# Kernel optimization log

Measured on AMD Instinct MI355X. Metric: run time of the kernel, lower is better.

Reference implementation:

```python
import jax, jax.numpy as jnp
import numpy as np

# PyTorch LSTM gate order: i, f, g, o. Dropout layers are identity in eval mode.

def _lstm_step(w_ih, w_hh, b):
    def step(carry, xt):
        h, c = carry
        g = xt @ w_ih.T + h @ w_hh.T + b
        i, f, gg, o = jnp.split(g, 4, axis=-1)
        c = jax.nn.sigmoid(f) * c + jax.nn.sigmoid(i) * jnp.tanh(gg)
        h = jax.nn.sigmoid(o) * jnp.tanh(c)
        return (h, c), h
    return step


def bilstm(x, wf_ih, wf_hh, bf_ih, bf_hh, wb_ih, wb_hh, bb_ih, bb_hh):
    # x: [B, T, D] -> out: [B, T, 2H]
    B = x.shape[0]
    H = wf_hh.shape[1]
    xt = jnp.swapaxes(x, 0, 1)  # [T, B, D]
    init = (jnp.zeros((B, H), x.dtype), jnp.zeros((B, H), x.dtype))
    _, hf = jax.lax.scan(_lstm_step(wf_ih, wf_hh, bf_ih + bf_hh), init, xt)
    _, hb = jax.lax.scan(_lstm_step(wb_ih, wb_hh, bb_ih + bb_hh), init, xt[::-1])
    hb = hb[::-1]
    return jnp.swapaxes(jnp.concatenate([hf, hb], axis=-1), 0, 1)


def setup_inputs() -> dict:
    key = jax.random.key(0)
    ks = iter(jax.random.split(key, 64))
    d = {"x": jax.random.normal(next(ks), (1024, 1024, 8), jnp.float32)}
    layer_dims = [(16, 20), (40, 20), (40, 10), (20, 10)]
    for li, (din, H) in enumerate(layer_dims, start=1):
        for dr in ("f", "b"):
            d[f"w{li}{dr}_ih"] = 0.1 * jax.random.normal(next(ks), (4 * H, din), jnp.float32)
            d[f"w{li}{dr}_hh"] = 0.1 * jax.random.normal(next(ks), (4 * H, H), jnp.float32)
            d[f"b{li}{dr}_ih"] = 0.1 * jax.random.normal(next(ks), (4 * H,), jnp.float32)
            d[f"b{li}{dr}_hh"] = 0.1 * jax.random.normal(next(ks), (4 * H,), jnp.float32)
    d["fc_w"] = 0.1 * jax.random.normal(next(ks), (1, 20), jnp.float32)
    d["fc_b"] = 0.1 * jax.random.normal(next(ks), (1,), jnp.float32)
    return d


def reference(x,
              w1f_ih, w1f_hh, b1f_ih, b1f_hh, w1b_ih, w1b_hh, b1b_ih, b1b_hh,
              w2f_ih, w2f_hh, b2f_ih, b2f_hh, w2b_ih, w2b_hh, b2b_ih, b2b_hh,
              w3f_ih, w3f_hh, b3f_ih, b3f_hh, w3b_ih, w3b_hh, b3b_ih, b3b_hh,
              w4f_ih, w4f_hh, b4f_ih, b4f_hh, w4b_ih, w4b_hh, b4b_ih, b4b_hh,
              fc_w, fc_b):
    # lag-1 concat: [B,T,8] -> [B,T,16]
    x_lag = jnp.concatenate([jnp.zeros_like(x[:, :1, :]), x[:, :-1, :]], axis=1)
    h = jnp.concatenate([x, x_lag], axis=2)
    h = bilstm(h, w1f_ih, w1f_hh, b1f_ih, b1f_hh, w1b_ih, w1b_hh, b1b_ih, b1b_hh)
    h = bilstm(h, w2f_ih, w2f_hh, b2f_ih, b2f_hh, w2b_ih, w2b_hh, b2b_ih, b2b_hh)
    h = bilstm(h, w3f_ih, w3f_hh, b3f_ih, b3f_hh, w3b_ih, w3b_hh, b3b_ih, b3b_hh)
    h = bilstm(h, w4f_ih, w4f_hh, b4f_ih, b4f_hh, w4b_ih, w4b_hh, b4b_ih, b4b_hh)
    h = h[:, -1, :]  # [B, 20]
    return jax.nn.sigmoid(h @ fc_w.T + fc_b)
```

## Files before the change

### kernel.cpp

```cpp
#include <hip/hip_runtime.h>
#include <hip/hip_fp16.h>
#include <stdint.h>

#define B_TOTAL 1024
#define T_TOTAL 1024
#define LOG2E 1.44269504088896f

typedef _Float16 f16x2 __attribute__((ext_vector_type(2)));

__device__ __forceinline__ float dot2acc(uint32_t xw, f16x2 w, float acc) {
#if __has_builtin(__builtin_amdgcn_fdot2)
    return __builtin_amdgcn_fdot2(__builtin_bit_cast(f16x2, xw), w, acc, false);
#else
    f16x2 xv = __builtin_bit_cast(f16x2, xw);
    return acc + (float)xv.x * (float)w.x + (float)xv.y * (float)w.y;
#endif
}

__device__ __forceinline__ uint32_t packf2(float a, float b) {
    f16x2 t;
    t.x = (_Float16)a;
    t.y = (_Float16)b;
    return __builtin_bit_cast(uint32_t, t);
}

__device__ __forceinline__ float sigm_(float z) {
    float e = __builtin_amdgcn_exp2f(-LOG2E * z);
    return __builtin_amdgcn_rcpf(1.0f + e);
}
__device__ __forceinline__ float tanh_(float z) {
    float e = __builtin_amdgcn_exp2f((2.0f * LOG2E) * z);
    float r = __builtin_amdgcn_rcpf(1.0f + e);
    return __builtin_fmaf(-2.0f, r, 1.0f);
}

__device__ __forceinline__ void wavebar() {
#if __has_builtin(__builtin_amdgcn_wave_barrier)
    __builtin_amdgcn_wave_barrier();
#endif
}

template <int DIN, int H, bool LAYER1, bool STORE_ALL>
__global__ void __launch_bounds__(64)
__attribute__((amdgpu_waves_per_eu(1, 1))) lstm_scan(
    const float* __restrict__ x,
    const __half* __restrict__ inbuf,
    const float* __restrict__ wihf, const float* __restrict__ whhf,
    const float* __restrict__ bihf, const float* __restrict__ bhhf,
    const float* __restrict__ wihb, const float* __restrict__ whhb,
    const float* __restrict__ bihb, const float* __restrict__ bhhb,
    __half* __restrict__ outbuf,
    float* __restrict__ lasth)
{
    constexpr int GPW   = 64 / H;
    constexpr int ND    = DIN / 2;
    constexpr int NH    = H / 2;
    constexpr int HS_DW = (H == 20) ? 12 : 8;

    const int dir  = blockIdx.y;
    const int lane = threadIdx.x;
    const int g    = lane / H;
    const int j    = lane - g * H;
    const int b    = blockIdx.x * GPW + g;
    const bool valid = (g < GPW) && (b < B_TOTAL);
    const int bs   = valid ? b : (B_TOTAL - 1);

    const float* w_ih = dir ? wihb : wihf;
    const float* w_hh = dir ? whhb : whhf;
    const float* b_ih = dir ? bihb : bihf;
    const float* b_hh = dir ? bhhb : bhhf;

    __shared__ uint32_t hsm[GPW + 1][HS_DW];

    f16x2 wih2[4][ND];
    f16x2 whh2[4][NH];
    float bias[4];
#pragma unroll
    for (int q = 0; q < 4; ++q) {
        const int r = q * H + j;
#pragma unroll
        for (int d = 0; d < ND; ++d) {
            f16x2 t;
            t.x = (_Float16)w_ih[r * DIN + 2 * d];
            t.y = (_Float16)w_ih[r * DIN + 2 * d + 1];
            wih2[q][d] = t;
        }
#pragma unroll
        for (int k = 0; k < NH; ++k) {
            f16x2 t;
            t.x = (_Float16)w_hh[r * H + 2 * k];
            t.y = (_Float16)w_hh[r * H + 2 * k + 1];
            whh2[q][k] = t;
        }
        bias[q] = b_ih[r] + b_hh[r];
    }

    const int tstep = dir ? -1 : 1;
    int tt = dir ? (T_TOTAL - 1) : 0;

    __half* op = nullptr;
    ptrdiff_t opstep = 0;
    if constexpr (STORE_ALL) {
        op = outbuf + (size_t)tt * (B_TOTAL * 2 * H) + (size_t)bs * (2 * H) + dir * H + j;
        opstep = (ptrdiff_t)tstep * (B_TOTAL * 2 * H);
    }

    float c = 0.0f;
    float hlast = 0.0f;
    ((__half*)&hsm[g][0])[j] = __float2half(0.0f);
    wavebar();

    auto tail = [&](const uint32_t* hd, float a0, float a1, float a2, float a3) {
#pragma unroll
        for (int k = 0; k < NH; ++k) {
            a0 = dot2acc(hd[k], whh2[0][k], a0);
            a1 = dot2acc(hd[k], whh2[1][k], a1);
            a2 = dot2acc(hd[k], whh2[2][k], a2);
            a3 = dot2acc(hd[k], whh2[3][k], a3);
        }
        const float iv = sigm_(a0);
        const float fv = sigm_(a1);
        const float gv = tanh_(a2);
        const float ov = sigm_(a3);
        c = __builtin_fmaf(fv, c, iv * gv);
        const float h = ov * tanh_(c);
        ((__half*)&hsm[g][0])[j] = __float2half(h);
        wavebar();
        if constexpr (STORE_ALL) {
            if (valid) *op = __float2half(h);
            op += opstep;
        } else {
            hlast = h;
        }
        tt += tstep;
    };

    if constexpr (LAYER1) {
        const float* xrow = x + (size_t)bs * (T_TOTAL * 8);
        uint32_t xcur[4], xlag[4];
        {
            const float4* p = (const float4*)(xrow + (size_t)tt * 8);
            float4 u0 = p[0], u1 = p[1];
            xcur[0] = packf2(u0.x, u0.y); xcur[1] = packf2(u0.z, u0.w);
            xcur[2] = packf2(u1.x, u1.y); xcur[3] = packf2(u1.z, u1.w);
            if (dir) {
                const float4* q = (const float4*)(xrow + (size_t)(tt - 1) * 8);
                float4 v0 = q[0], v1 = q[1];
                xlag[0] = packf2(v0.x, v0.y); xlag[1] = packf2(v0.z, v0.w);
                xlag[2] = packf2(v1.x, v1.y); xlag[3] = packf2(v1.z, v1.w);
            } else {
#pragma unroll
                for (int d = 0; d < 4; ++d) xlag[d] = 0u;
            }
        }

        for (int t = 0; t < T_TOTAL; ++t) {
            uint32_t hd[NH];
#pragma unroll
            for (int k = 0; k < NH; ++k) hd[k] = hsm[g][k];

            float a0 = bias[0], a1 = bias[1], a2 = bias[2], a3 = bias[3];
#pragma unroll
            for (int d = 0; d < 4; ++d) {
                a0 = dot2acc(xcur[d], wih2[0][d], a0);
                a1 = dot2acc(xcur[d], wih2[1][d], a1);
                a2 = dot2acc(xcur[d], wih2[2][d], a2);
                a3 = dot2acc(xcur[d], wih2[3][d], a3);
            }
#pragma unroll
            for (int d = 0; d < 4; ++d) {
                a0 = dot2acc(xlag[d], wih2[0][4 + d], a0);
                a1 = dot2acc(xlag[d], wih2[1][4 + d], a1);
                a2 = dot2acc(xlag[d], wih2[2][4 + d], a2);
                a3 = dot2acc(xlag[d], wih2[3][4 + d], a3);
            }

            const int li = dir ? (tt - 2) : (tt + 1);
            const bool ld = (li >= 0) && (li < T_TOTAL);
            float4 n0 = {0, 0, 0, 0}, n1 = {0, 0, 0, 0};
            if (ld) {
                const float4* p = (const float4*)(xrow + (size_t)li * 8);
                n0 = p[0];
                n1 = p[1];
            }

            tail(hd, a0, a1, a2, a3);

            uint32_t np[4] = {packf2(n0.x, n0.y), packf2(n0.z, n0.w),
                              packf2(n1.x, n1.y), packf2(n1.z, n1.w)};
            if (dir == 0) {
#pragma unroll
                for (int d = 0; d < 4; ++d) { xlag[d] = xcur[d]; xcur[d] = np[d]; }
            } else {
#pragma unroll
                for (int d = 0; d < 4; ++d) {
                    xcur[d] = xlag[d];
                    xlag[d] = ld ? np[d] : 0u;
                }
            }
        }
    } else {
        const ptrdiff_t ipstep = (ptrdiff_t)tstep * (B_TOTAL * ND);
        const uint32_t* ip = (const uint32_t*)inbuf + (size_t)tt * (B_TOTAL * ND) + (size_t)bs * ND;

        uint32_t xb[4][ND];
#pragma unroll
        for (int s = 0; s < 3; ++s) {
#pragma unroll
            for (int d = 0; d < ND; ++d) xb[s][d] = ip[d];
            ip += ipstep;
        }

        auto step = [&](const uint32_t* xc, uint32_t* xn, bool pf) {
            uint32_t hd[NH];
#pragma unroll
            for (int k = 0; k < NH; ++k) hd[k] = hsm[g][k];

            float a0 = bias[0], a1 = bias[1], a2 = bias[2], a3 = bias[3];
#pragma unroll
            for (int d = 0; d < ND; ++d) {
                a0 = dot2acc(xc[d], wih2[0][d], a0);
                a1 = dot2acc(xc[d], wih2[1][d], a1);
                a2 = dot2acc(xc[d], wih2[2][d], a2);
                a3 = dot2acc(xc[d], wih2[3][d], a3);
            }
            if (pf) {
#pragma unroll
                for (int d = 0; d < ND; ++d) xn[d] = ip[d];
                ip += ipstep;
            }
            tail(hd, a0, a1, a2, a3);
        };

        for (int t = 0; t < T_TOTAL; t += 4) {
            step(xb[0], xb[3], t + 3 < T_TOTAL);
            step(xb[1], xb[0], t + 4 < T_TOTAL);
            step(xb[2], xb[1], t + 5 < T_TOTAL);
            step(xb[3], xb[2], t + 6 < T_TOTAL);
        }
    }

    if constexpr (!STORE_ALL) {
        if (valid) lasth[b * H + j] = hlast;
    }
}

__global__ void final_kernel(const __half* __restrict__ l3out,
                             const float* __restrict__ hf4,
                             const float* __restrict__ w_ih,
                             const float* __restrict__ b_ih,
                             const float* __restrict__ b_hh,
                             const float* __restrict__ fc_w,
                             const float* __restrict__ fc_b,
                             float* __restrict__ out)
{
    const int b = blockIdx.x * blockDim.x + threadIdx.x;
    if (b >= B_TOTAL) return;

    float in4[20];
    const __half* p = l3out + (size_t)(T_TOTAL - 1) * (B_TOTAL * 20) + (size_t)b * 20;
#pragma unroll
    for (int i = 0; i < 20; ++i) in4[i] = __half2float(p[i]);

    float z = fc_b[0];
#pragma unroll
    for (int k = 0; k < 10; ++k) z += fc_w[k] * hf4[b * 10 + k];

#pragma unroll
    for (int k = 0; k < 10; ++k) {
        float gi = b_ih[k]      + b_hh[k];
        float gg = b_ih[20 + k] + b_hh[20 + k];
        float go = b_ih[30 + k] + b_hh[30 + k];
#pragma unroll
        for (int i = 0; i < 20; ++i) {
            const float xi = in4[i];
            gi += w_ih[k * 20 + i]        * xi;
            gg += w_ih[(20 + k) * 20 + i] * xi;
            go += w_ih[(30 + k) * 20 + i] * xi;
        }
        const float cc = sigm_(gi) * tanh_(gg);
        const float hb = sigm_(go) * tanh_(cc);
        z += fc_w[10 + k] * hb;
    }
    out[b] = sigm_(z);
}

extern "C" void kernel_launch(void* const* d_in, const int* in_sizes, int n_in,
                              void* d_out, int out_size, void* d_ws, size_t ws_size,
                              hipStream_t stream) {
    const float* x = (const float*)d_in[0];
    auto W = [&](int li, int dr, int k) -> const float* {
        return (const float*)d_in[1 + (li - 1) * 8 + dr * 4 + k];
    };
    const float* fc_w = (const float*)d_in[33];
    const float* fc_b = (const float*)d_in[34];
    float* out = (float*)d_out;

    __half* buf0 = (__half*)d_ws;
    __half* buf1 = buf0 + (size_t)T_TOTAL * B_TOTAL * 40;
    float* hf4 = (float*)(buf1 + (size_t)T_TOTAL * B_TOTAL * 40);

    lstm_scan<16, 20, true, true><<<dim3(342, 2, 1), 64, 0, stream>>>(
        x, nullptr,
        W(1,0,0), W(1,0,1), W(1,0,2), W(1,0,3),
        W(1,1,0), W(1,1,1), W(1,1,2), W(1,1,3),
        buf0, nullptr);

    lstm_scan<40, 20, false, true><<<dim3(342, 2, 1), 64, 0, stream>>>(
        nullptr, buf0,
        W(2,0,0), W(2,0,1), W(2,0,2), W(2,0,3),
        W(2,1,0), W(2,1,1), W(2,1,2), W(2,1,3),
        buf1, nullptr);

    lstm_scan<40, 10, false, true><<<dim3(171, 2, 1), 64, 0, stream>>>(
        nullptr, buf1,
        W(3,0,0), W(3,0,1), W(3,0,2), W(3,0,3),
        W(3,1,0), W(3,1,1), W(3,1,2), W(3,1,3),
        buf0, nullptr);

    lstm_scan<20, 10, false, false><<<dim3(171, 1, 1), 64, 0, stream>>>(
        nullptr, buf0,
        W(4,0,0), W(4,0,1), W(4,0,2), W(4,0,3),
        W(4,0,0), W(4,0,1), W(4,0,2), W(4,0,3),
        nullptr, hf4);

    final_kernel<<<dim3(4, 1, 1), 256, 0, stream>>>(
        buf0, hf4, W(4,1,0), W(4,1,2), W(4,1,3), fc_w, fc_b, out);
}
```

Measured before the change: 1.739 ms.

## Stage LSTM inputs through double-buffered LDS chunks with coalesced block loads

Replaces the per-lane strided global loads of each timestep's input with chunked cooperative loads. The whole wave fetches CHUNK timesteps into registers, writes them to a double-buffered shared-memory tile mid-chunk, and each lane reads its row from LDS one step ahead. The aim is coalesced global traffic and global load latency hidden off the serial recurrence. It also keeps weights as packed uint32 pinned with empty asm. This adds LDS usage, extra registers for the staging buffer, and indexing arithmetic inside the critical loop.

```diff
diff --git a/kernel.cpp b/kernel.cpp
--- a/kernel.cpp
+++ b/kernel.cpp
@@ -8,12 +8,14 @@
 
 typedef _Float16 f16x2 __attribute__((ext_vector_type(2)));
 
-__device__ __forceinline__ float dot2acc(uint32_t xw, f16x2 w, float acc) {
+__device__ __forceinline__ float dot2w(uint32_t xw, uint32_t ww, float acc) {
 #if __has_builtin(__builtin_amdgcn_fdot2)
-    return __builtin_amdgcn_fdot2(__builtin_bit_cast(f16x2, xw), w, acc, false);
+    return __builtin_amdgcn_fdot2(__builtin_bit_cast(f16x2, xw),
+                                  __builtin_bit_cast(f16x2, ww), acc, false);
 #else
     f16x2 xv = __builtin_bit_cast(f16x2, xw);
-    return acc + (float)xv.x * (float)w.x + (float)xv.y * (float)w.y;
+    f16x2 wv = __builtin_bit_cast(f16x2, ww);
+    return acc + (float)xv.x * (float)wv.x + (float)xv.y * (float)wv.y;
 #endif
 }
 
@@ -52,10 +54,16 @@
     __half* __restrict__ outbuf,
     float* __restrict__ lasth)
 {
-    constexpr int GPW   = 64 / H;
-    constexpr int ND    = DIN / 2;
-    constexpr int NH    = H / 2;
-    constexpr int HS_DW = (H == 20) ? 12 : 8;
+    constexpr int GPW    = 64 / H;
+    constexpr int ND     = DIN / 2;
+    constexpr int NH     = H / 2;
+    constexpr int HS_DW  = (H == 20) ? 12 : 8;
+    constexpr int CHUNK  = (GPW == 3) ? 16 : 8;
+    constexpr int NCHUNK = T_TOTAL / CHUNK;
+    constexpr int NDX    = LAYER1 ? 4 : ND;
+    constexpr int XROWS  = LAYER1 ? (CHUNK + 1) : CHUNK;
+    constexpr int XWORDS = XROWS * GPW * NDX;
+    constexpr int NLOAD  = (XWORDS + 63) / 64;
 
     const int dir  = blockIdx.y;
     const int lane = threadIdx.x;
@@ -70,30 +78,89 @@
     const float* b_ih = dir ? bihb : bihf;
     const float* b_hh = dir ? bhhb : bhhf;
 
+    __shared__ uint32_t xsm[2 * XWORDS];
     __shared__ uint32_t hsm[GPW + 1][HS_DW];
 
-    f16x2 wih2[4][ND];
-    f16x2 whh2[4][NH];
+    uint32_t wih2[4][ND];
+    uint32_t whh2[4][NH];
     float bias[4];
 #pragma unroll
     for (int q = 0; q < 4; ++q) {
         const int r = q * H + j;
 #pragma unroll
-        for (int d = 0; d < ND; ++d) {
-            f16x2 t;
-            t.x = (_Float16)w_ih[r * DIN + 2 * d];
-            t.y = (_Float16)w_ih[r * DIN + 2 * d + 1];
-            wih2[q][d] = t;
-        }
-#pragma unroll
-        for (int k = 0; k < NH; ++k) {
-            f16x2 t;
-            t.x = (_Float16)w_hh[r * H + 2 * k];
-            t.y = (_Float16)w_hh[r * H + 2 * k + 1];
-            whh2[q][k] = t;
-        }
+        for (int d = 0; d < ND; ++d)
+            wih2[q][d] = packf2(w_ih[r * DIN + 2 * d], w_ih[r * DIN + 2 * d + 1]);
+#pragma unroll
+        for (int k = 0; k < NH; ++k)
+            whh2[q][k] = packf2(w_hh[r * H + 2 * k], w_hh[r * H + 2 * k + 1]);
         bias[q] = b_ih[r] + b_hh[r];
     }
+#pragma unroll
+    for (int q = 0; q < 4; ++q) {
+#pragma unroll
+        for (int d = 0; d < ND; ++d) asm volatile("" : "+v"(wih2[q][d]));
+#pragma unroll
+        for (int k = 0; k < NH; ++k) asm volatile("" : "+v"(whh2[q][k]));
+        asm volatile("" : "+v"(bias[q]));
+    }
+
+    uint32_t greg[NLOAD];
+
+    auto stage_load = [&](int c) {
+        const int sbase = c * CHUNK;
+#pragma unroll
+        for (int i = 0; i < NLOAD; ++i) {
+            const int idx = lane + 64 * i;
+            uint32_t v = 0;
+            if (idx < XWORDS) {
+                const int row = idx / (GPW * NDX);
+                const int rem = idx - row * (GPW * NDX);
+                const int r   = rem / NDX;
+                const int d   = rem - r * NDX;
+                const int br  = blockIdx.x * GPW + r;
+                int t;
+                if constexpr (LAYER1)
+                    t = dir ? (T_TOTAL - 1 - sbase) - row : (sbase - 1) + row;
+                else
+                    t = dir ? (T_TOTAL - 1) - (sbase + row) : sbase + row;
+                if (t >= 0 && t < T_TOTAL && br < B_TOTAL) {
+                    if constexpr (LAYER1) {
+                        const float2 p = ((const float2*)(x + (size_t)br * (T_TOTAL * 8) +
+                                                          (size_t)t * 8))[d];
+                        v = packf2(p.x, p.y);
+                    } else {
+                        v = ((const uint32_t*)inbuf)[(size_t)t * (B_TOTAL * ND) +
+                                                     (size_t)br * ND + d];
+                    }
+                }
+            }
+            greg[i] = v;
+        }
+    };
+    auto stage_write = [&](int buf) {
+#pragma unroll
+        for (int i = 0; i < NLOAD; ++i) {
+            const int idx = lane + 64 * i;
+            if (idx < XWORDS) xsm[buf * XWORDS + idx] = greg[i];
+        }
+    };
+
+    auto xread = [&](int buf, int row, uint32_t* dst) {
+        const uint32_t* p = &xsm[buf * XWORDS + row * (GPW * NDX) + g * NDX];
+        if constexpr (NDX % 4 == 0) {
+#pragma unroll
+            for (int d = 0; d < NDX; d += 4) {
+                uint4 v = *(const uint4*)(p + d);
+                dst[d] = v.x; dst[d + 1] = v.y; dst[d + 2] = v.z; dst[d + 3] = v.w;
+            }
+        } else {
+#pragma unroll
+            for (int d = 0; d < NDX; d += 2) {
+                uint2 v = *(const uint2*)(p + d);
+                dst[d] = v.x; dst[d + 1] = v.y;
+            }
+        }
+    };
 
     const int tstep = dir ? -1 : 1;
     int tt = dir ? (T_TOTAL - 1) : 0;
@@ -105,25 +172,28 @@
         opstep = (ptrdiff_t)tstep * (B_TOTAL * 2 * H);
     }
 
-    float c = 0.0f;
+    float c_st = 0.0f;
     float hlast = 0.0f;
     ((__half*)&hsm[g][0])[j] = __float2half(0.0f);
     wavebar();
 
+    stage_load(0);
+    stage_write(0);
+
     auto tail = [&](const uint32_t* hd, float a0, float a1, float a2, float a3) {
 #pragma unroll
         for (int k = 0; k < NH; ++k) {
-            a0 = dot2acc(hd[k], whh2[0][k], a0);
-            a1 = dot2acc(hd[k], whh2[1][k], a1);
-            a2 = dot2acc(hd[k], whh2[2][k], a2);
-            a3 = dot2acc(hd[k], whh2[3][k], a3);
+            a0 = dot2w(hd[k], whh2[0][k], a0);
+            a1 = dot2w(hd[k], whh2[1][k], a1);
+            a2 = dot2w(hd[k], whh2[2][k], a2);
+            a3 = dot2w(hd[k], whh2[3][k], a3);
         }
         const float iv = sigm_(a0);
         const float fv = sigm_(a1);
         const float gv = tanh_(a2);
         const float ov = sigm_(a3);
-        c = __builtin_fmaf(fv, c, iv * gv);
-        const float h = ov * tanh_(c);
+        c_st = __builtin_fmaf(fv, c_st, iv * gv);
+        const float h = ov * tanh_(c_st);
         ((__half*)&hsm[g][0])[j] = __float2half(h);
         wavebar();
         if constexpr (STORE_ALL) {
@@ -136,107 +206,87 @@
     };
 
     if constexpr (LAYER1) {
-        const float* xrow = x + (size_t)bs * (T_TOTAL * 8);
-        uint32_t xcur[4], xlag[4];
-        {
-            const float4* p = (const float4*)(xrow + (size_t)tt * 8);
-            float4 u0 = p[0], u1 = p[1];
-            xcur[0] = packf2(u0.x, u0.y); xcur[1] = packf2(u0.z, u0.w);
-            xcur[2] = packf2(u1.x, u1.y); xcur[3] = packf2(u1.z, u1.w);
-            if (dir) {
-                const float4* q = (const float4*)(xrow + (size_t)(tt - 1) * 8);
-                float4 v0 = q[0], v1 = q[1];
-                xlag[0] = packf2(v0.x, v0.y); xlag[1] = packf2(v0.z, v0.w);
-                xlag[2] = packf2(v1.x, v1.y); xlag[3] = packf2(v1.z, v1.w);
-            } else {
-#pragma unroll
-                for (int d = 0; d < 4; ++d) xlag[d] = 0u;
-            }
-        }
-
-        for (int t = 0; t < T_TOTAL; ++t) {
-            uint32_t hd[NH];
-#pragma unroll
-            for (int k = 0; k < NH; ++k) hd[k] = hsm[g][k];
-
-            float a0 = bias[0], a1 = bias[1], a2 = bias[2], a3 = bias[3];
-#pragma unroll
-            for (int d = 0; d < 4; ++d) {
-                a0 = dot2acc(xcur[d], wih2[0][d], a0);
-                a1 = dot2acc(xcur[d], wih2[1][d], a1);
-                a2 = dot2acc(xcur[d], wih2[2][d], a2);
-                a3 = dot2acc(xcur[d], wih2[3][d], a3);
-            }
-#pragma unroll
-            for (int d = 0; d < 4; ++d) {
-                a0 = dot2acc(xlag[d], wih2[0][4 + d], a0);
-                a1 = dot2acc(xlag[d], wih2[1][4 + d], a1);
-                a2 = dot2acc(xlag[d], wih2[2][4 + d], a2);
-                a3 = dot2acc(xlag[d], wih2[3][4 + d], a3);
-            }
-
-            const int li = dir ? (tt - 2) : (tt + 1);
-            const bool ld = (li >= 0) && (li < T_TOTAL);
-            float4 n0 = {0, 0, 0, 0}, n1 = {0, 0, 0, 0};
-            if (ld) {
-                const float4* p = (const float4*)(xrow + (size_t)li * 8);
-                n0 = p[0];
-                n1 = p[1];
-            }
-
-            tail(hd, a0, a1, a2, a3);
-
-            uint32_t np[4] = {packf2(n0.x, n0.y), packf2(n0.z, n0.w),
-                              packf2(n1.x, n1.y), packf2(n1.z, n1.w)};
-            if (dir == 0) {
-#pragma unroll
-                for (int d = 0; d < 4; ++d) { xlag[d] = xcur[d]; xcur[d] = np[d]; }
-            } else {
+        uint32_t cur4[4], lag4[4], nrow[4];
+        xread(0, dir ? 0 : 1, cur4);
+        xread(0, dir ? 1 : 0, lag4);
+
+        int buf = 0;
+        for (int c = 0; c < NCHUNK; ++c) {
+#pragma unroll
+            for (int k = 0; k < CHUNK; ++k) {
+                uint32_t hd[NH];
+#pragma unroll
+                for (int q = 0; q < NH; ++q) hd[q] = hsm[g][q];
+
+                if (k == 0 && c + 1 < NCHUNK) stage_load(c + 1);
+
+                float a0 = bias[0], a1 = bias[1], a2 = bias[2], a3 = bias[3];
 #pragma unroll
                 for (int d = 0; d < 4; ++d) {
-                    xcur[d] = xlag[d];
-                    xlag[d] = ld ? np[d] : 0u;
-                }
-            }
+                    a0 = dot2w(cur4[d], wih2[0][d], a0);
+                    a1 = dot2w(cur4[d], wih2[1][d], a1);
+                    a2 = dot2w(cur4[d], wih2[2][d], a2);
+                    a3 = dot2w(cur4[d], wih2[3][d], a3);
+                }
+#pragma unroll
+                for (int d = 0; d < 4; ++d) {
+                    a0 = dot2w(lag4[d], wih2[0][4 + d], a0);
+                    a1 = dot2w(lag4[d], wih2[1][4 + d], a1);
+                    a2 = dot2w(lag4[d], wih2[2][4 + d], a2);
+                    a3 = dot2w(lag4[d], wih2[3][4 + d], a3);
+                }
+
+                if (k < CHUNK - 1) xread(buf, k + 2, nrow);
+                else               xread(buf ^ 1, 1, nrow);
+
+                if (k == CHUNK / 2 && c + 1 < NCHUNK) stage_write(buf ^ 1);
+
+                tail(hd, a0, a1, a2, a3);
+
+                if (dir == 0) {
+#pragma unroll
+                    for (int d = 0; d < 4; ++d) { lag4[d] = cur4[d]; cur4[d] = nrow[d]; }
+                } else {
+#pragma unroll
+                    for (int d = 0; d < 4; ++d) { cur4[d] = lag4[d]; lag4[d] = nrow[d]; }
+                }
+            }
+            buf ^= 1;
         }
     } else {
-        const ptrdiff_t ipstep = (ptrdiff_t)tstep * (B_TOTAL * ND);
-        const uint32_t* ip = (const uint32_t*)inbuf + (size_t)tt * (B_TOTAL * ND) + (size_t)bs * ND;
-
-        uint32_t xb[4][ND];
-#pragma unroll
-        for (int s = 0; s < 3; ++s) {
-#pragma unroll
-            for (int d = 0; d < ND; ++d) xb[s][d] = ip[d];
-            ip += ipstep;
-        }
-
-        auto step = [&](const uint32_t* xc, uint32_t* xn, bool pf) {
-            uint32_t hd[NH];
-#pragma unroll
-            for (int k = 0; k < NH; ++k) hd[k] = hsm[g][k];
-
-            float a0 = bias[0], a1 = bias[1], a2 = bias[2], a3 = bias[3];
-#pragma unroll
-            for (int d = 0; d < ND; ++d) {
-                a0 = dot2acc(xc[d], wih2[0][d], a0);
-                a1 = dot2acc(xc[d], wih2[1][d], a1);
-                a2 = dot2acc(xc[d], wih2[2][d], a2);
-                a3 = dot2acc(xc[d], wih2[3][d], a3);
-            }
-            if (pf) {
-#pragma unroll
-                for (int d = 0; d < ND; ++d) xn[d] = ip[d];
-                ip += ipstep;
-            }
-            tail(hd, a0, a1, a2, a3);
-        };
-
-        for (int t = 0; t < T_TOTAL; t += 4) {
-            step(xb[0], xb[3], t + 3 < T_TOTAL);
-            step(xb[1], xb[0], t + 4 < T_TOTAL);
-            step(xb[2], xb[1], t + 5 < T_TOTAL);
-            step(xb[3], xb[2], t + 6 < T_TOTAL);
+        uint32_t xcA[ND], xcB[ND];
+        xread(0, 0, xcA);
+
+        int buf = 0;
+        for (int c = 0; c < NCHUNK; ++c) {
+#pragma unroll
+            for (int k = 0; k < CHUNK; ++k) {
+                const uint32_t* xc = (k & 1) ? xcB : xcA;
+                uint32_t*       xn = (k & 1) ? xcA : xcB;
+
+                uint32_t hd[NH];
+#pragma unroll
+                for (int q = 0; q < NH; ++q) hd[q] = hsm[g][q];
+
+                if (k == 0 && c + 1 < NCHUNK) stage_load(c + 1);
+
+                float a0 = bias[0], a1 = bias[1], a2 = bias[2], a3 = bias[3];
+#pragma unroll
+                for (int d = 0; d < ND; ++d) {
+                    a0 = dot2w(xc[d], wih2[0][d], a0);
+                    a1 = dot2w(xc[d], wih2[1][d], a1);
+                    a2 = dot2w(xc[d], wih2[2][d], a2);
+                    a3 = dot2w(xc[d], wih2[3][d], a3);
+                }
+
+                if (k < CHUNK - 1) xread(buf, k + 1, xn);
+                else               xread(buf ^ 1, 0, xn);
+
+                if (k == CHUNK / 2 && c + 1 < NCHUNK) stage_write(buf ^ 1);
+
+                tail(hd, a0, a1, a2, a3);
+            }
+            buf ^= 1;
         }
     }
 
```

Result: faster. 1.665 ms (-4.2%).

## Hoist LSTM input projections into separate parallel GEMM kernels over time segments

Applied to the files above, without the earlier changes.

Splits each layer into a parallel proj_kernel that precomputes the input-to-gate projections (x·W_ih) for a time segment into an fp16 workspace buffer. A slimmer lstm_scan2 then only does the recurrent h·W_hh part, with an 8-deep prefetch of the gate inputs and state carried across segments through global h/c buffers. The aim is to shorten the serial per-step critical path by moving the input matmul off it. In exchange it adds extra global memory traffic and more kernel launches. Segment length depends on workspace size, and gate pre-activations are rounded to fp16, which may reduce accuracy.

```diff
diff --git a/kernel.cpp b/kernel.cpp
--- a/kernel.cpp
+++ b/kernel.cpp
@@ -8,12 +8,14 @@
 
 typedef _Float16 f16x2 __attribute__((ext_vector_type(2)));
 
-__device__ __forceinline__ float dot2acc(uint32_t xw, f16x2 w, float acc) {
+__device__ __forceinline__ float dot2w(uint32_t xw, uint32_t ww, float acc) {
 #if __has_builtin(__builtin_amdgcn_fdot2)
-    return __builtin_amdgcn_fdot2(__builtin_bit_cast(f16x2, xw), w, acc, false);
+    return __builtin_amdgcn_fdot2(__builtin_bit_cast(f16x2, xw),
+                                  __builtin_bit_cast(f16x2, ww), acc, false);
 #else
     f16x2 xv = __builtin_bit_cast(f16x2, xw);
-    return acc + (float)xv.x * (float)w.x + (float)xv.y * (float)w.y;
+    f16x2 wv = __builtin_bit_cast(f16x2, ww);
+    return acc + (float)xv.x * (float)wv.x + (float)xv.y * (float)wv.y;
 #endif
 }
 
@@ -40,22 +42,122 @@
 #endif
 }
 
-template <int DIN, int H, bool LAYER1, bool STORE_ALL>
-__global__ void __launch_bounds__(64)
-__attribute__((amdgpu_waves_per_eu(1, 1))) lstm_scan(
+template <int DIN, int H, int NDIR, bool L1X>
+__global__ void __launch_bounds__(256) proj_kernel(
     const float* __restrict__ x,
     const __half* __restrict__ inbuf,
-    const float* __restrict__ wihf, const float* __restrict__ whhf,
-    const float* __restrict__ bihf, const float* __restrict__ bhhf,
-    const float* __restrict__ wihb, const float* __restrict__ whhb,
-    const float* __restrict__ bihb, const float* __restrict__ bhhb,
+    const float* __restrict__ w0,
+    const float* __restrict__ w1,
+    __half* __restrict__ g0,
+    __half* __restrict__ g1,
+    int t0, int seglen)
+{
+    constexpr int NDW = DIN / 2;
+    constexpr int O4H = 4 * H;
+    constexpr int ODW = O4H / 2;
+    constexpr int RPB = 16;
+    constexpr int TPR = 16;
+    constexpr int OPT = (O4H + TPR - 1) / TPR;
+    constexpr int TILES = 8;
+
+    __shared__ uint32_t wt[NDW][O4H];
+    __shared__ uint32_t xin[RPB * NDW];
+    __shared__ uint32_t osm[RPB][ODW];
+
+    const int tid  = threadIdx.x;
+    const int dirz = (NDIR == 2) ? (int)blockIdx.y : 0;
+    const float* w = dirz ? w1 : w0;
+    __half* gout   = dirz ? g1 : g0;
+    (void)seglen;
+
+    for (int idx = tid; idx < NDW * O4H; idx += 256) {
+        const int d  = idx / O4H;
+        const int o  = idx - d * O4H;
+        const int jj = o >> 2;
+        const int qq = o & 3;
+        wt[d][o] = packf2(w[(qq * H + jj) * DIN + 2 * d],
+                          w[(qq * H + jj) * DIN + 2 * d + 1]);
+    }
+
+    const int rr = tid >> 4;
+    const int li = tid & 15;
+
+    for (int tile = 0; tile < TILES; ++tile) {
+        const int r0 = ((int)blockIdx.x * TILES + tile) * RPB;
+        __syncthreads();
+
+        for (int idx = tid; idx < RPB * NDW; idx += 256) {
+            const int r  = r0 + idx / NDW;
+            const int d  = idx % NDW;
+            const int i  = r >> 10;
+            const int bb = r & (B_TOTAL - 1);
+            const int t  = dirz ? (T_TOTAL - 1 - t0 - i) : (t0 + i);
+            uint32_t v;
+            if constexpr (L1X) {
+                float2 u = {0.f, 0.f};
+                if (d < 4)
+                    u = ((const float2*)(x + ((size_t)bb * T_TOTAL + t) * 8))[d];
+                else if (t > 0)
+                    u = ((const float2*)(x + ((size_t)bb * T_TOTAL + (t - 1)) * 8))[d - 4];
+                v = packf2(u.x, u.y);
+            } else {
+                v = ((const uint32_t*)inbuf)[((size_t)t * B_TOTAL + bb) * NDW + d];
+            }
+            xin[idx] = v;
+        }
+        __syncthreads();
+
+        float acc[OPT];
+#pragma unroll
+        for (int oi = 0; oi < OPT; ++oi) acc[oi] = 0.f;
+#pragma unroll
+        for (int d = 0; d < NDW; ++d) {
+            const uint32_t xv = xin[rr * NDW + d];
+#pragma unroll
+            for (int oi = 0; oi < OPT; ++oi) {
+                const int o = li + oi * TPR;
+                if (O4H % TPR == 0 || o < O4H)
+                    acc[oi] = dot2w(xv, wt[d][o], acc[oi]);
+            }
+        }
+        {
+            __half* oh = (__half*)&osm[rr][0];
+#pragma unroll
+            for (int oi = 0; oi < OPT; ++oi) {
+                const int o = li + oi * TPR;
+                if (O4H % TPR == 0 || o < O4H) oh[o] = __float2half(acc[oi]);
+            }
+        }
+        __syncthreads();
+
+        {
+            uint32_t* dst = (uint32_t*)gout;
+            for (int idx = tid; idx < RPB * ODW; idx += 256) {
+                const int r  = idx / ODW;
+                const int od = idx - r * ODW;
+                dst[(size_t)(r0 + r) * ODW + od] = osm[r][od];
+            }
+        }
+    }
+}
+
+template <int H, bool STORE_ALL>
+__global__ void __launch_bounds__(64)
+__attribute__((amdgpu_waves_per_eu(1, 1))) lstm_scan2(
+    const __half* __restrict__ gxf, const __half* __restrict__ gxb,
+    const float* __restrict__ whhf, const float* __restrict__ bihf,
+    const float* __restrict__ bhhf,
+    const float* __restrict__ whhb, const float* __restrict__ bihb,
+    const float* __restrict__ bhhb,
     __half* __restrict__ outbuf,
-    float* __restrict__ lasth)
+    float* __restrict__ lasth,
+    float* __restrict__ sth, float* __restrict__ stc,
+    int t0, int seglen)
 {
     constexpr int GPW   = 64 / H;
-    constexpr int ND    = DIN / 2;
     constexpr int NH    = H / 2;
     constexpr int HS_DW = (H == 20) ? 12 : 8;
+    constexpr int PF    = 8;
 
     const int dir  = blockIdx.y;
     const int lane = threadIdx.x;
@@ -65,183 +167,123 @@
     const bool valid = (g < GPW) && (b < B_TOTAL);
     const int bs   = valid ? b : (B_TOTAL - 1);
 
-    const float* w_ih = dir ? wihb : wihf;
+    const __half* gx  = dir ? gxb : gxf;
     const float* w_hh = dir ? whhb : whhf;
-    const float* b_ih = dir ? bihb : bihf;
-    const float* b_hh = dir ? bhhb : bhhf;
+    const float* b_i  = dir ? bihb : bihf;
+    const float* b_h  = dir ? bhhb : bhhf;
 
     __shared__ uint32_t hsm[GPW + 1][HS_DW];
 
-    f16x2 wih2[4][ND];
-    f16x2 whh2[4][NH];
+    uint32_t whh2[4][NH];
     float bias[4];
 #pragma unroll
     for (int q = 0; q < 4; ++q) {
         const int r = q * H + j;
 #pragma unroll
-        for (int d = 0; d < ND; ++d) {
-            f16x2 t;
-            t.x = (_Float16)w_ih[r * DIN + 2 * d];
-            t.y = (_Float16)w_ih[r * DIN + 2 * d + 1];
-            wih2[q][d] = t;
-        }
-#pragma unroll
-        for (int k = 0; k < NH; ++k) {
-            f16x2 t;
-            t.x = (_Float16)w_hh[r * H + 2 * k];
-            t.y = (_Float16)w_hh[r * H + 2 * k + 1];
-            whh2[q][k] = t;
-        }
-        bias[q] = b_ih[r] + b_hh[r];
-    }
-
-    const int tstep = dir ? -1 : 1;
-    int tt = dir ? (T_TOTAL - 1) : 0;
+        for (int k = 0; k < NH; ++k)
+            whh2[q][k] = packf2(w_hh[r * H + 2 * k], w_hh[r * H + 2 * k + 1]);
+        bias[q] = b_i[r] + b_h[r];
+    }
+#pragma unroll
+    for (int q = 0; q < 4; ++q) {
+#pragma unroll
+        for (int k = 0; k < NH; ++k) asm volatile("" : "+v"(whh2[q][k]));
+        asm volatile("" : "+v"(bias[q]));
+    }
+
+    float c_st, h0;
+    if (t0 == 0) {
+        c_st = 0.f;
+        h0   = 0.f;
+    } else {
+        h0   = sth[((size_t)dir * B_TOTAL + bs) * H + j];
+        c_st = stc[((size_t)dir * B_TOTAL + bs) * H + j];
+    }
+    ((__half*)&hsm[g][0])[j] = __float2half(h0);
+    wavebar();
+
+    uint32_t hd[NH];
+    auto readhd = [&]() {
+        const uint32_t* hp = &hsm[g][0];
+        if constexpr (NH == 10) {
+            uint4 v0 = *(const uint4*)hp;
+            uint4 v1 = *(const uint4*)(hp + 4);
+            uint2 v2 = *(const uint2*)(hp + 8);
+            hd[0] = v0.x; hd[1] = v0.y; hd[2] = v0.z; hd[3] = v0.w;
+            hd[4] = v1.x; hd[5] = v1.y; hd[6] = v1.z; hd[7] = v1.w;
+            hd[8] = v2.x; hd[9] = v2.y;
+        } else {
+            uint4 v0 = *(const uint4*)hp;
+            hd[0] = v0.x; hd[1] = v0.y; hd[2] = v0.z; hd[3] = v0.w;
+            hd[4] = hp[4];
+        }
+    };
+    readhd();
+
+    const char*  gb   = (const char*)gx + ((size_t)bs * (4 * H) + (size_t)j * 4) * 2;
+    const size_t ISTR = (size_t)B_TOTAL * (4 * H) * 2;
+
+    uint2 pf[PF];
+#pragma unroll
+    for (int i2 = 0; i2 < PF; ++i2) {
+        const int ip = (i2 < seglen) ? i2 : (seglen - 1);
+        pf[i2] = *(const uint2*)(gb + (size_t)ip * ISTR);
+    }
 
     __half* op = nullptr;
     ptrdiff_t opstep = 0;
     if constexpr (STORE_ALL) {
-        op = outbuf + (size_t)tt * (B_TOTAL * 2 * H) + (size_t)bs * (2 * H) + dir * H + j;
-        opstep = (ptrdiff_t)tstep * (B_TOTAL * 2 * H);
-    }
-
-    float c = 0.0f;
-    float hlast = 0.0f;
-    ((__half*)&hsm[g][0])[j] = __float2half(0.0f);
-    wavebar();
-
-    auto tail = [&](const uint32_t* hd, float a0, float a1, float a2, float a3) {
-#pragma unroll
-        for (int k = 0; k < NH; ++k) {
-            a0 = dot2acc(hd[k], whh2[0][k], a0);
-            a1 = dot2acc(hd[k], whh2[1][k], a1);
-            a2 = dot2acc(hd[k], whh2[2][k], a2);
-            a3 = dot2acc(hd[k], whh2[3][k], a3);
-        }
-        const float iv = sigm_(a0);
-        const float fv = sigm_(a1);
-        const float gv = tanh_(a2);
-        const float ov = sigm_(a3);
-        c = __builtin_fmaf(fv, c, iv * gv);
-        const float h = ov * tanh_(c);
-        ((__half*)&hsm[g][0])[j] = __float2half(h);
-        wavebar();
-        if constexpr (STORE_ALL) {
-            if (valid) *op = __float2half(h);
-            op += opstep;
-        } else {
-            hlast = h;
-        }
-        tt += tstep;
-    };
-
-    if constexpr (LAYER1) {
-        const float* xrow = x + (size_t)bs * (T_TOTAL * 8);
-        uint32_t xcur[4], xlag[4];
-        {
-            const float4* p = (const float4*)(xrow + (size_t)tt * 8);
-            float4 u0 = p[0], u1 = p[1];
-            xcur[0] = packf2(u0.x, u0.y); xcur[1] = packf2(u0.z, u0.w);
-            xcur[2] = packf2(u1.x, u1.y); xcur[3] = packf2(u1.z, u1.w);
-            if (dir) {
-                const float4* q = (const float4*)(xrow + (size_t)(tt - 1) * 8);
-                float4 v0 = q[0], v1 = q[1];
-                xlag[0] = packf2(v0.x, v0.y); xlag[1] = packf2(v0.z, v0.w);
-                xlag[2] = packf2(v1.x, v1.y); xlag[3] = packf2(v1.z, v1.w);
-            } else {
-#pragma unroll
-                for (int d = 0; d < 4; ++d) xlag[d] = 0u;
-            }
-        }
-
-        for (int t = 0; t < T_TOTAL; ++t) {
-            uint32_t hd[NH];
-#pragma unroll
-            for (int k = 0; k < NH; ++k) hd[k] = hsm[g][k];
-
-            float a0 = bias[0], a1 = bias[1], a2 = bias[2], a3 = bias[3];
-#pragma unroll
-            for (int d = 0; d < 4; ++d) {
-                a0 = dot2acc(xcur[d], wih2[0][d], a0);
-                a1 = dot2acc(xcur[d], wih2[1][d], a1);
-                a2 = dot2acc(xcur[d], wih2[2][d], a2);
-                a3 = dot2acc(xcur[d], wih2[3][d], a3);
-            }
-#pragma unroll
-            for (int d = 0; d < 4; ++d) {
-                a0 = dot2acc(xlag[d], wih2[0][4 + d], a0);
-                a1 = dot2acc(xlag[d], wih2[1][4 + d], a1);
-                a2 = dot2acc(xlag[d], wih2[2][4 + d], a2);
-                a3 = dot2acc(xlag[d], wih2[3][4 + d], a3);
-            }
-
-            const int li = dir ? (tt - 2) : (tt + 1);
-            const bool ld = (li >= 0) && (li < T_TOTAL);
-            float4 n0 = {0, 0, 0, 0}, n1 = {0, 0, 0, 0};
-            if (ld) {
-                const float4* p = (const float4*)(xrow + (size_t)li * 8);
-                n0 = p[0];
-                n1 = p[1];
-            }
-
-            tail(hd, a0, a1, a2, a3);
-
-            uint32_t np[4] = {packf2(n0.x, n0.y), packf2(n0.z, n0.w),
-                              packf2(n1.x, n1.y), packf2(n1.z, n1.w)};
-            if (dir == 0) {
-#pragma unroll
-                for (int d = 0; d < 4; ++d) { xlag[d] = xcur[d]; xcur[d] = np[d]; }
-            } else {
-#pragma unroll
-                for (int d = 0; d < 4; ++d) {
-                    xcur[d] = xlag[d];
-                    xlag[d] = ld ? np[d] : 0u;
-                }
-            }
-        }
-    } else {
-        const ptrdiff_t ipstep = (ptrdiff_t)tstep * (B_TOTAL * ND);
-        const uint32_t* ip = (const uint32_t*)inbuf + (size_t)tt * (B_TOTAL * ND) + (size_t)bs * ND;
-
-        uint32_t xb[4][ND];
-#pragma unroll
-        for (int s = 0; s < 3; ++s) {
-#pragma unroll
-            for (int d = 0; d < ND; ++d) xb[s][d] = ip[d];
-            ip += ipstep;
-        }
-
-        auto step = [&](const uint32_t* xc, uint32_t* xn, bool pf) {
-            uint32_t hd[NH];
-#pragma unroll
-            for (int k = 0; k < NH; ++k) hd[k] = hsm[g][k];
-
-            float a0 = bias[0], a1 = bias[1], a2 = bias[2], a3 = bias[3];
-#pragma unroll
-            for (int d = 0; d < ND; ++d) {
-                a0 = dot2acc(xc[d], wih2[0][d], a0);
-                a1 = dot2acc(xc[d], wih2[1][d], a1);
-                a2 = dot2acc(xc[d], wih2[2][d], a2);
-                a3 = dot2acc(xc[d], wih2[3][d], a3);
-            }
-            if (pf) {
-#pragma unroll
-                for (int d = 0; d < ND; ++d) xn[d] = ip[d];
-                ip += ipstep;
-            }
-            tail(hd, a0, a1, a2, a3);
-        };
-
-        for (int t = 0; t < T_TOTAL; t += 4) {
-            step(xb[0], xb[3], t + 3 < T_TOTAL);
-            step(xb[1], xb[0], t + 4 < T_TOTAL);
-            step(xb[2], xb[1], t + 5 < T_TOTAL);
-            step(xb[3], xb[2], t + 6 < T_TOTAL);
-        }
-    }
-
-    if constexpr (!STORE_ALL) {
-        if (valid) lasth[b * H + j] = hlast;
+        const int tstart = dir ? (T_TOTAL - 1 - t0) : t0;
+        op = outbuf + (size_t)tstart * (B_TOTAL * 2 * H) + (size_t)bs * (2 * H) + dir * H + j;
+        opstep = (dir ? -1 : 1) * (ptrdiff_t)(B_TOTAL * 2 * H);
+    }
+
+    float hlast = h0;
+
+#define STEP(I)                                                               \
+    {                                                                         \
+        const uint2 gv = pf[I];                                               \
+        int ip = sb + (I) + PF;                                               \
+        ip = (ip < seglen) ? ip : (seglen - 1);                               \
+        pf[I] = *(const uint2*)(gb + (size_t)ip * ISTR);                      \
+        const f16x2 p01 = __builtin_bit_cast(f16x2, gv.x);                    \
+        const f16x2 p23 = __builtin_bit_cast(f16x2, gv.y);                    \
+        float a0 = (float)p01.x + bias[0];                                    \
+        float a1 = (float)p01.y + bias[1];                                    \
+        float a2 = (float)p23.x + bias[2];                                    \
+        float a3 = (float)p23.y + bias[3];                                    \
+        _Pragma("unroll")                                                     \
+        for (int k = 0; k < NH; ++k) {                                        \
+            a0 = dot2w(hd[k], whh2[0][k], a0);                                \
+            a1 = dot2w(hd[k], whh2[1][k], a1);                                \
+            a2 = dot2w(hd[k], whh2[2][k], a2);                                \
+            a3 = dot2w(hd[k], whh2[3][k], a3);                                \
+        }                                                                     \
+        const float iv = sigm_(a0);                                           \
+        const float fv = sigm_(a1);                                           \
+        const float gv2 = tanh_(a2);                                          \
+        const float ov = sigm_(a3);                                           \
+        c_st = __builtin_fmaf(fv, c_st, iv * gv2);                            \
+        const float h = ov * tanh_(c_st);                                     \
+        ((__half*)&hsm[g][0])[j] = __float2half(h);                           \
+        wavebar();                                                            \
+        readhd();                                                             \
+        hlast = h;                                                            \
+        if constexpr (STORE_ALL) {                                            \
+            if (valid) *op = __float2half(h);                                 \
+            op += opstep;                                                     \
+        }                                                                     \
+    }
+
+    for (int sb = 0; sb < seglen; sb += PF) {
+        STEP(0) STEP(1) STEP(2) STEP(3) STEP(4) STEP(5) STEP(6) STEP(7)
+    }
+#undef STEP
+
+    if (valid) {
+        sth[((size_t)dir * B_TOTAL + b) * H + j] = hlast;
+        stc[((size_t)dir * B_TOTAL + b) * H + j] = c_st;
+        if constexpr (!STORE_ALL) lasth[b * H + j] = hlast;
     }
 }
 
@@ -296,34 +338,62 @@
     const float* fc_b = (const float*)d_in[34];
     float* out = (float*)d_out;
 
-    __half* buf0 = (__half*)d_ws;
-    __half* buf1 = buf0 + (size_t)T_TOTAL * B_TOTAL * 40;
-    float* hf4 = (float*)(buf1 + (size_t)T_TOTAL * B_TOTAL * 40);
-
-    lstm_scan<16, 20, true, true><<<dim3(342, 2, 1), 64, 0, stream>>>(
-        x, nullptr,
-        W(1,0,0), W(1,0,1), W(1,0,2), W(1,0,3),
-        W(1,1,0), W(1,1,1), W(1,1,2), W(1,1,3),
-        buf0, nullptr);
-
-    lstm_scan<40, 20, false, true><<<dim3(342, 2, 1), 64, 0, stream>>>(
-        nullptr, buf0,
-        W(2,0,0), W(2,0,1), W(2,0,2), W(2,0,3),
-        W(2,1,0), W(2,1,1), W(2,1,2), W(2,1,3),
-        buf1, nullptr);
-
-    lstm_scan<40, 10, false, true><<<dim3(171, 2, 1), 64, 0, stream>>>(
-        nullptr, buf1,
-        W(3,0,0), W(3,0,1), W(3,0,2), W(3,0,3),
-        W(3,1,0), W(3,1,1), W(3,1,2), W(3,1,3),
-        buf0, nullptr);
-
-    lstm_scan<20, 10, false, false><<<dim3(171, 1, 1), 64, 0, stream>>>(
-        nullptr, buf0,
-        W(4,0,0), W(4,0,1), W(4,0,2), W(4,0,3),
-        W(4,0,0), W(4,0,1), W(4,0,2), W(4,0,3),
-        nullptr, hf4);
-
-    final_kernel<<<dim3(4, 1, 1), 256, 0, stream>>>(
-        buf0, hf4, W(4,1,0), W(4,1,2), W(4,1,3), fc_w, fc_b, out);
-}
+    const size_t HA_B = (size_t)T_TOTAL * B_TOTAL * 40 * 2;
+    const size_t HB_B = (size_t)T_TOTAL * B_TOTAL * 20 * 2;
+    const size_t ST_B = 2ull * B_TOTAL * 20 * 4;
+    const size_t F4_B = (size_t)B_TOTAL * 10 * 4;
+
+    char* p = (char*)d_ws;
+    __half* hA = (__half*)p;  p += HA_B;
+    __half* hB = (__half*)p;  p += HB_B;
+    float* sth = (float*)p;   p += ST_B;
+    float* stc = (float*)p;   p += ST_B;
+    float* hf4 = (float*)p;   p += F4_B;
+    __half* gx = (__half*)p;
+
+    const size_t base = HA_B + HB_B + 2 * ST_B + F4_B;
+    int SEG = 64;
+    if      (ws_size >= base + 1024ull * 327680) SEG = 1024;
+    else if (ws_size >= base +  512ull * 327680) SEG = 512;
+    else if (ws_size >= base +  256ull * 327680) SEG = 256;
+    else if (ws_size >= base +  128ull * 327680) SEG = 128;
+    const int nseg = T_TOTAL / SEG;
+
+    auto g1of = [&](int H) { return gx + (size_t)SEG * 1024 * 4 * H; };
+
+    for (int s = 0; s < nseg; ++s) {
+        proj_kernel<16, 20, 2, true><<<dim3(SEG * 8, 2), 256, 0, stream>>>(
+            x, nullptr, W(1,0,0), W(1,1,0), gx, g1of(20), s * SEG, SEG);
+        lstm_scan2<20, true><<<dim3(342, 2), 64, 0, stream>>>(
+            gx, g1of(20), W(1,0,1), W(1,0,2), W(1,0,3),
+                          W(1,1,1), W(1,1,2), W(1,1,3),
+            hA, nullptr, sth, stc, s * SEG, SEG);
+    }
+    for (int s = 0; s < nseg; ++s) {
+        proj_kernel<40, 20, 2, false><<<dim3(SEG * 8, 2), 256, 0, stream>>>(
+            nullptr, hA, W(2,0,0), W(2,1,0), gx, g1of(20), s * SEG, SEG);
+        lstm_scan2<20, true><<<dim3(342, 2), 64, 0, stream>>>(
+            gx, g1of(20), W(2,0,1), W(2,0,2), W(2,0,3),
+                          W(2,1,1), W(2,1,2), W(2,1,3),
+            hA, nullptr, sth, stc, s * SEG, SEG);
+    }
+    for (int s = 0; s < nseg; ++s) {
+        proj_kernel<40, 10, 2, false><<<dim3(SEG * 8, 2), 256, 0, stream>>>(
+            nullptr, hA, W(3,0,0), W(3,1,0), gx, g1of(10), s * SEG, SEG);
+        lstm_scan2<10, true><<<dim3(171, 2), 64, 0, stream>>>(
+            gx, g1of(10), W(3,0,1), W(3,0,2), W(3,0,3),
+                          W(3,1,1), W(3,1,2), W(3,1,3),
+            hB, nullptr, sth, stc, s * SEG, SEG);
+    }
+    for (int s = 0; s < nseg; ++s) {
+        proj_kernel<20, 10, 1, false><<<dim3(SEG * 8, 1), 256, 0, stream>>>(
+            nullptr, hB, W(4,0,0), W(4,0,0), gx, gx, s * SEG, SEG);
+        lstm_scan2<10, false><<<dim3(171, 1), 64, 0, stream>>>(
+            gx, gx, W(4,0,1), W(4,0,2), W(4,0,3),
+                    W(4,0,1), W(4,0,2), W(4,0,3),
+            nullptr, hf4, sth, stc, s * SEG, SEG);
+    }
+
+    final_kernel<<<dim3(4), 256, 0, stream>>>(
+        hB, hf4, W(4,1,0), W(4,1,2), W(4,1,3), fc_w, fc_b, out);
+}
```

Measured after the change: 1.801 ms. +3.6%, slower.
